# Performance work log

Hardware: AMD Instinct MI355X
Metric: run time of the kernel (lower is better)

Reference implementation:

```python
import jax, jax.numpy as jnp
import numpy as np

COMMITMENT_COST = 0.25


def setup_inputs() -> dict:
    key = jax.random.key(0)
    k1, k2 = jax.random.split(key)
    x = jax.random.normal(k1, (4, 64, 32, 32, 32), dtype=jnp.float32)
    weight = jax.random.normal(k2, (512, 64), dtype=jnp.float32)
    return {"x": x, "weight": weight}


def reference(x, weight):
    b, c, h, w, d = x.shape  # c == embed_dim
    # [b, h, w, d, c] -> [N, c]
    flat = jnp.transpose(x, (0, 2, 3, 4, 1)).reshape(-1, c)
    # squared L2 distances to each codebook vector: [N, n_embed]
    distances = (
        jnp.sum(flat * flat, axis=1, keepdims=True)
        - 2.0 * (flat @ weight.T)
        + jnp.sum(weight * weight, axis=1)
    )
    embed_idx_flat = jnp.argmin(distances, axis=1)  # == argmax(-distances)
    embed_idx = embed_idx_flat.reshape(b, h, w, d)
    # gather codebook rows and move embed dim back to channel position
    quantized = jnp.transpose(weight[embed_idx], (0, 4, 1, 2, 3))  # [b, c, h, w, d]
    latent_loss = COMMITMENT_COST * jnp.mean(
        (jax.lax.stop_gradient(quantized) - x) ** 2
    )
    quantized_st = jax.lax.stop_gradient(quantized - x) + x
    return quantized_st, embed_idx, latent_loss
```

## Files before the change

kernel.cpp:

```cpp
#include <hip/hip_runtime.h>
#include <hip/hip_bf16.h>

#define HWD      32768
#define NC       64
#define NE       512
#define OUT_IDX  8388608
#define OUT_LOSS 8519680

#define WS_WSQ_F   16
#define WS_SLOT_F  528
#define WS_WP_B    4096
#define WS_NEEDED  200704

typedef __attribute__((ext_vector_type(8))) short bf16x8;
typedef __attribute__((ext_vector_type(4))) float f32x4;

__device__ inline unsigned short bf16_rne(float v) {
    unsigned u = __builtin_bit_cast(unsigned, v);
    return (unsigned short)((u + 0x7FFFu + ((u >> 16) & 1u)) >> 16);
}
__device__ inline float bf16_f(unsigned short s) {
    return __builtin_bit_cast(float, (unsigned)s << 16);
}
__device__ inline void split3(float v, unsigned short& h, unsigned short& m,
                              unsigned short& l) {
    h = bf16_rne(v);
    float r1 = v - bf16_f(h);
    m = bf16_rne(r1);
    float r2 = r1 - bf16_f(m);
    l = bf16_rne(r2);
}

__global__ __launch_bounds__(256) void vq_prep(
    const float* __restrict__ w, float* __restrict__ ws)
{
    const int gtid = blockIdx.x * 256 + threadIdx.x;
    if (gtid == 0) { ws[0] = 0.f; ((unsigned*)ws)[1] = 0u; }
    if (gtid < 256) ws[WS_SLOT_F + gtid] = 0.f;
    if (gtid < NE) {
        const float4* row = (const float4*)(w + (size_t)gtid * NC);
        float s0 = 0.f, s1 = 0.f, s2 = 0.f, s3 = 0.f;
#pragma unroll
        for (int k = 0; k < 16; ++k) {
            float4 v = row[k];
            s0 = fmaf(v.x, v.x, s0); s1 = fmaf(v.y, v.y, s1);
            s2 = fmaf(v.z, v.z, s2); s3 = fmaf(v.w, v.w, s3);
        }
        ws[WS_WSQ_F + gtid] = (s0 + s1) + (s2 + s3);
    }
    const int lane_s = gtid & 63;
    int t = gtid >> 6;
    const int plane = t % 3; t /= 3;
    const int kc = t & 1;
    const int ct = t >> 1;
    const int code = ct * 16 + (lane_s & 15);
    const int kb   = kc * 32 + (lane_s >> 4) * 8;
    const float* src = w + (size_t)code * NC + kb;
    unsigned short o[8];
#pragma unroll
    for (int j = 0; j < 8; ++j) {
        unsigned short h, m, l;
        split3(src[j], h, m, l);
        o[j] = (plane == 0) ? h : (plane == 1) ? m : l;
    }
    unsigned short* dst = (unsigned short*)((char*)ws + WS_WP_B) + (size_t)gtid * 8;
#pragma unroll
    for (int j = 0; j < 8; ++j) dst[j] = o[j];
}

__device__ __forceinline__ void tileUpdPt(const bf16x8 (&Apt)[2][3],
                                          const bf16x8 (&B)[2][3],
                                          const float wsq, const int ct,
                                          const int lanelo,
                                          float (&best)[4], int (&bidx)[4])
{
    f32x4 acc = {0.f, 0.f, 0.f, 0.f};
    acc = __builtin_amdgcn_mfma_f32_16x16x32_bf16(Apt[0][2], B[0][0], acc, 0, 0, 0);
    acc = __builtin_amdgcn_mfma_f32_16x16x32_bf16(Apt[1][2], B[1][0], acc, 0, 0, 0);
    acc = __builtin_amdgcn_mfma_f32_16x16x32_bf16(Apt[0][1], B[0][1], acc, 0, 0, 0);
    acc = __builtin_amdgcn_mfma_f32_16x16x32_bf16(Apt[1][1], B[1][1], acc, 0, 0, 0);
    acc = __builtin_amdgcn_mfma_f32_16x16x32_bf16(Apt[0][0], B[0][2], acc, 0, 0, 0);
    acc = __builtin_amdgcn_mfma_f32_16x16x32_bf16(Apt[1][0], B[1][2], acc, 0, 0, 0);
    acc = __builtin_amdgcn_mfma_f32_16x16x32_bf16(Apt[0][1], B[0][0], acc, 0, 0, 0);
    acc = __builtin_amdgcn_mfma_f32_16x16x32_bf16(Apt[1][1], B[1][0], acc, 0, 0, 0);
    acc = __builtin_amdgcn_mfma_f32_16x16x32_bf16(Apt[0][0], B[0][1], acc, 0, 0, 0);
    acc = __builtin_amdgcn_mfma_f32_16x16x32_bf16(Apt[1][0], B[1][1], acc, 0, 0, 0);
    acc = __builtin_amdgcn_mfma_f32_16x16x32_bf16(Apt[0][0], B[0][0], acc, 0, 0, 0);
    acc = __builtin_amdgcn_mfma_f32_16x16x32_bf16(Apt[1][0], B[1][0], acc, 0, 0, 0);
#pragma unroll
    for (int r = 0; r < 4; ++r) {
        const float d = fmaf(-2.f, acc[r], wsq);
        if (d < best[r]) { best[r] = d; bidx[r] = ct * 16 + lanelo; }
    }
}

__global__ __launch_bounds__(256, 2) void vq_argmin(
    const float* __restrict__ x, float* __restrict__ ws,
    float* __restrict__ out)
{
    __shared__ int   idx_sh[256];
    __shared__ __align__(16) char Bsh[4][6144];
    __shared__ float wsq_sh[NE];

    const int tid    = threadIdx.x;
    const int wv     = tid >> 6;
    const int lane   = tid & 63;
    const int lanelo = lane & 15;
    const int quad   = lane >> 4;
    const int posB   = blockIdx.x * 256;
    const int b      = posB >> 15;
    const int hwdB   = posB & (HWD - 1);
    const size_t xoff = (size_t)b * NC * HWD + hwdB;
    const int wpos   = wv * 64;

    const char*  wpB  = (const char*)ws + WS_WP_B;
    const float* wsqp = ws + WS_WSQ_F;

    auto stageB = [&](int t, int bsel) {
#pragma unroll
        for (int cc = 0; cc < 2; ++cc) {
            const int c = wv + 4 * cc;
            if (c < 6) {
                const char* g = wpB + ((size_t)(t * 6 + c) * 64 + lane) * 16;
                void* l = &Bsh[bsel][c * 1024];
                __builtin_amdgcn_global_load_lds(
                    (const __attribute__((address_space(1))) unsigned*)g,
                    (__attribute__((address_space(3))) unsigned*)l, 16, 0, 0);
            }
        }
    };

    stageB(0, 0);
    stageB(1, 1);
    { wsq_sh[tid] = wsqp[tid]; wsq_sh[tid + 256] = wsqp[tid + 256]; }

    bf16x8 A[4][2][3];
#pragma unroll
    for (int pt = 0; pt < 4; ++pt) {
#pragma unroll
        for (int kc = 0; kc < 2; ++kc) {
            bf16x8 fh, fm, fl;
#pragma unroll
            for (int j = 0; j < 8; ++j) {
                const int k = kc * 32 + quad * 8 + j;
                const float v = x[xoff + (size_t)k * HWD + wpos + pt * 16 + lanelo];
                unsigned short h, m, l;
                split3(v, h, m, l);
                fh[j] = (short)h; fm[j] = (short)m; fl[j] = (short)l;
            }
            A[pt][kc][0] = fh; A[pt][kc][1] = fm; A[pt][kc][2] = fl;
        }
    }

    float best[4][4];
    int   bidx[4][4];
#pragma unroll
    for (int pt = 0; pt < 4; ++pt)
#pragma unroll
        for (int r = 0; r < 4; ++r) { best[pt][r] = 3.402823466e38f; bidx[pt][r] = 0; }

    __syncthreads();

#pragma unroll 1
    for (int r = 0; r < 16; ++r) {
        const int base = (r & 1) * 2;
        if (r < 15) {
            stageB(2 * r + 2, base ^ 2);
            stageB(2 * r + 3, (base ^ 2) + 1);
        }
#pragma unroll
        for (int s = 0; s < 2; ++s) {
            const int t = 2 * r + s;
            bf16x8 B[2][3];
            const bf16x8* bb = (const bf16x8*)Bsh[base + s];
#pragma unroll
            for (int kc = 0; kc < 2; ++kc)
#pragma unroll
                for (int p = 0; p < 3; ++p)
                    B[kc][p] = bb[(kc * 3 + p) * 64 + lane];
            const float wsq_c = wsq_sh[t * 16 + lanelo];
#pragma unroll
            for (int pt = 0; pt < 4; ++pt)
                tileUpdPt(A[pt], B, wsq_c, t, lanelo, best[pt], bidx[pt]);
        }
        __syncthreads();
    }

#pragma unroll
    for (int pt = 0; pt < 4; ++pt)
#pragma unroll
        for (int r = 0; r < 4; ++r) {
            float d = best[pt][r]; int i = bidx[pt][r];
#pragma unroll
            for (int mlane = 1; mlane <= 8; mlane <<= 1) {
                const float d2 = __shfl_xor(d, mlane);
                const int   i2 = __shfl_xor(i, mlane);
                if (d2 < d || (d2 == d && i2 < i)) { d = d2; i = i2; }
            }
            if (lanelo == 0)
                idx_sh[wpos + pt * 16 + quad * 4 + r] = i;
        }
    __syncthreads();

    out[OUT_IDX + posB + tid] = (float)idx_sh[tid];
}

__global__ __launch_bounds__(256, 8) void vq_epilogue(
    const float* __restrict__ x, const float* __restrict__ w,
    float* __restrict__ ws, float* __restrict__ out)
{
    __shared__ float q_t[64 * 68];
    __shared__ int   idx_sh[64];
    __shared__ float wred[4];

    const int tid  = threadIdx.x;
    const int posB = blockIdx.x * 64;
    const int b    = posB >> 15;
    const int hwdB = posB & (HWD - 1);
    const size_t xoff = (size_t)b * NC * HWD + hwdB;

    if (tid < 64) idx_sh[tid] = (int)out[OUT_IDX + posB + tid];
    __syncthreads();

#pragma unroll
    for (int it = 0; it < 16; ++it) {
        const int e = it * 256 + tid;
        const int r = e >> 6, c = e & 63;
        q_t[c * 68 + r] = w[(size_t)idx_sh[r] * NC + c];
    }
    __syncthreads();

    float lsum = 0.f;
#pragma unroll
    for (int it = 0; it < 4; ++it) {
        const int s  = it * 256 + tid;
        const int c  = s >> 4;
        const int p0 = (s & 15) * 4;
        const size_t off = xoff + (size_t)c * HWD + p0;
        const float4 xv = *(const float4*)(x + off);
        const float4 qv = *(const float4*)(q_t + c * 68 + p0);
        const float dx = qv.x - xv.x, dy = qv.y - xv.y;
        const float dz = qv.z - xv.z, dw = qv.w - xv.w;
        lsum = fmaf(dx, dx, lsum); lsum = fmaf(dy, dy, lsum);
        lsum = fmaf(dz, dz, lsum); lsum = fmaf(dw, dw, lsum);
        float4 ov;
        ov.x = dx + xv.x; ov.y = dy + xv.y;
        ov.z = dz + xv.z; ov.w = dw + xv.w;
        *(float4*)(out + off) = ov;
    }

#pragma unroll
    for (int off = 32; off >= 1; off >>= 1) lsum += __shfl_down(lsum, off);
    if ((tid & 63) == 0) wred[tid >> 6] = lsum;
    __syncthreads();
    if (tid == 0)
        atomicAdd(ws + WS_SLOT_F + (blockIdx.x & 255),
                  (wred[0] + wred[1]) + (wred[2] + wred[3]));
}

__global__ __launch_bounds__(64) void vq_loss_fin(
    const float* __restrict__ ws, float* __restrict__ out)
{
    const int lane = threadIdx.x;
    float s = (ws[WS_SLOT_F + lane]       + ws[WS_SLOT_F + lane + 64]) +
              (ws[WS_SLOT_F + lane + 128] + ws[WS_SLOT_F + lane + 192]);
#pragma unroll
    for (int off = 32; off >= 1; off >>= 1) s += __shfl_down(s, off);
    if (lane == 0) out[OUT_LOSS] = 0.25f * s / 8388608.0f;
}

__global__ __launch_bounds__(256, 2) void vq_fused_fb(
    const float* __restrict__ x, const float* __restrict__ w,
    float* __restrict__ out, float* __restrict__ loss_acc)
{
    __shared__ float lw[256 * NC];
    __shared__ float wsq[256];
    __shared__ float wred[4];
    const int tid = threadIdx.x;
    const int n0  = blockIdx.x * 512;
    const int b   = n0 >> 15;
    const int hwd = (n0 & (HWD - 1)) + tid;
    const float* xp = x + (size_t)b * NC * HWD + hwd;
    float xr0[NC], xr1[NC];
#pragma unroll
    for (int c = 0; c < NC; ++c) { xr0[c] = xp[(size_t)c * HWD]; xr1[c] = xp[(size_t)c * HWD + 256]; }
    float xsq0 = 0.f, xsq1 = 0.f;
#pragma unroll
    for (int c = 0; c < NC; ++c) { xsq0 = fmaf(xr0[c], xr0[c], xsq0); xsq1 = fmaf(xr1[c], xr1[c], xsq1); }
    float best0 = 3.402823466e38f, best1 = 3.402823466e38f;
    int bi0 = 0, bi1 = 0;
    for (int pass = 0; pass < 2; ++pass) {
        if (pass) __syncthreads();
        const float4* wt = (const float4*)(w + pass * 256 * NC);
        float4* l4 = (float4*)lw;
#pragma unroll
        for (int k = 0; k < 16; ++k) l4[tid + k * 256] = wt[tid + k * 256];
        {
            const float4* row = wt + tid * 16;
            float s0 = 0.f, s1 = 0.f, s2 = 0.f, s3 = 0.f;
#pragma unroll
            for (int k = 0; k < 16; ++k) {
                float4 v = row[k];
                s0 = fmaf(v.x, v.x, s0); s1 = fmaf(v.y, v.y, s1);
                s2 = fmaf(v.z, v.z, s2); s3 = fmaf(v.w, v.w, s3);
            }
            wsq[tid] = (s0 + s1) + (s2 + s3);
        }
        __syncthreads();
#pragma unroll 2
        for (int e = 0; e < 256; ++e) {
            const float4* row = (const float4*)(lw + e * NC);
            float a0 = 0.f, a1 = 0.f, c0 = 0.f, c1 = 0.f;
#pragma unroll
            for (int k = 0; k < 16; ++k) {
                float4 v = row[k];
                a0 = fmaf(xr0[4 * k + 0], v.x, a0); a1 = fmaf(xr0[4 * k + 1], v.y, a1);
                a0 = fmaf(xr0[4 * k + 2], v.z, a0); a1 = fmaf(xr0[4 * k + 3], v.w, a1);
                c0 = fmaf(xr1[4 * k + 0], v.x, c0); c1 = fmaf(xr1[4 * k + 1], v.y, c1);
                c0 = fmaf(xr1[4 * k + 2], v.z, c0); c1 = fmaf(xr1[4 * k + 3], v.w, c1);
            }
            const float d0 = (xsq0 - 2.f * (a0 + a1)) + wsq[e];
            const float d1 = (xsq1 - 2.f * (c0 + c1)) + wsq[e];
            const int ge = pass * 256 + e;
            if (d0 < best0) { best0 = d0; bi0 = ge; }
            if (d1 < best1) { best1 = d1; bi1 = ge; }
        }
    }
    float* o0 = out + (size_t)b * NC * HWD + hwd;
    float lsum = 0.f;
    const float4* r0 = (const float4*)(w + bi0 * NC);
    const float4* r1 = (const float4*)(w + bi1 * NC);
#pragma unroll
    for (int k = 0; k < 16; ++k) {
        float4 q0 = r0[k], q1 = r1[k];
        float qv0[4] = { q0.x, q0.y, q0.z, q0.w };
        float qv1[4] = { q1.x, q1.y, q1.z, q1.w };
#pragma unroll
        for (int j = 0; j < 4; ++j) {
            const int c = 4 * k + j;
            const float dv0 = qv0[j] - xr0[c];
            const float dv1 = qv1[j] - xr1[c];
            lsum = fmaf(dv0, dv0, lsum); lsum = fmaf(dv1, dv1, lsum);
            o0[(size_t)c * HWD] = dv0 + xr0[c];
            o0[(size_t)c * HWD + 256] = dv1 + xr1[c];
        }
    }
    const int n = b * HWD + hwd;
    out[OUT_IDX + n] = (float)bi0;
    out[OUT_IDX + n + 256] = (float)bi1;
#pragma unroll
    for (int off = 32; off >= 1; off >>= 1) lsum += __shfl_down(lsum, off);
    if ((tid & 63) == 0) wred[tid >> 6] = lsum;
    __syncthreads();
    if (tid == 0) atomicAdd(loss_acc, (wred[0] + wred[1]) + (wred[2] + wred[3]));
}

__global__ void vq_loss_fin_fb(const float* __restrict__ acc, float* __restrict__ out)
{
    out[OUT_LOSS] = 0.25f * acc[0] / 8388608.0f;
}

extern "C" void kernel_launch(void* const* d_in, const int* in_sizes, int n_in,
                              void* d_out, int out_size, void* d_ws, size_t ws_size,
                              hipStream_t stream)
{
    const float* x = (const float*)d_in[0];
    const float* w = (const float*)d_in[1];
    float* out = (float*)d_out;
    float* ws  = (float*)d_ws;

    if (ws_size >= WS_NEEDED) {
        vq_prep<<<48, 256, 0, stream>>>(w, ws);
        vq_argmin<<<512, 256, 0, stream>>>(x, ws, out);
        vq_epilogue<<<2048, 256, 0, stream>>>(x, w, ws, out);
        vq_loss_fin<<<1, 64, 0, stream>>>(ws, out);
    } else {
        hipMemsetAsync(d_ws, 0, sizeof(float), stream);
        vq_fused_fb<<<256, 256, 0, stream>>>(x, w, out, ws);
        vq_loss_fin_fb<<<1, 1, 0, stream>>>(ws, out);
    }
}
```

Baseline: 136.0 us.

## Load codebook fragments directly to registers and interleave MFMA chains across point tiles

Drops the LDS staging of the split-bf16 codebook (global_load_lds with double buffering and per-iteration barriers). Each wave now loads its B fragments and wsq straight from global/L2 into registers, software-pipelined one code tile ahead. The MFMA loop is also restructured so that four independent accumulator chains (one per point tile) are interleaved, which hides MFMA dependency latency. In exchange there are more redundant global loads per wave, since every wave fetches the same codebook data, and register pressure rises under launch bounds of two blocks per SM.

New measurement: 135.3 us (median of 3 runs). No clear change (-0.5%).

```diff
diff --git a/kernel.cpp b/kernel.cpp
--- a/kernel.cpp
+++ b/kernel.cpp
@@ -68,39 +68,53 @@
     for (int j = 0; j < 8; ++j) dst[j] = o[j];
 }
 
-__device__ __forceinline__ void tileUpdPt(const bf16x8 (&Apt)[2][3],
-                                          const bf16x8 (&B)[2][3],
-                                          const float wsq, const int ct,
-                                          const int lanelo,
-                                          float (&best)[4], int (&bidx)[4])
-{
-    f32x4 acc = {0.f, 0.f, 0.f, 0.f};
-    acc = __builtin_amdgcn_mfma_f32_16x16x32_bf16(Apt[0][2], B[0][0], acc, 0, 0, 0);
-    acc = __builtin_amdgcn_mfma_f32_16x16x32_bf16(Apt[1][2], B[1][0], acc, 0, 0, 0);
-    acc = __builtin_amdgcn_mfma_f32_16x16x32_bf16(Apt[0][1], B[0][1], acc, 0, 0, 0);
-    acc = __builtin_amdgcn_mfma_f32_16x16x32_bf16(Apt[1][1], B[1][1], acc, 0, 0, 0);
-    acc = __builtin_amdgcn_mfma_f32_16x16x32_bf16(Apt[0][0], B[0][2], acc, 0, 0, 0);
-    acc = __builtin_amdgcn_mfma_f32_16x16x32_bf16(Apt[1][0], B[1][2], acc, 0, 0, 0);
-    acc = __builtin_amdgcn_mfma_f32_16x16x32_bf16(Apt[0][1], B[0][0], acc, 0, 0, 0);
-    acc = __builtin_amdgcn_mfma_f32_16x16x32_bf16(Apt[1][1], B[1][0], acc, 0, 0, 0);
-    acc = __builtin_amdgcn_mfma_f32_16x16x32_bf16(Apt[0][0], B[0][1], acc, 0, 0, 0);
-    acc = __builtin_amdgcn_mfma_f32_16x16x32_bf16(Apt[1][0], B[1][1], acc, 0, 0, 0);
-    acc = __builtin_amdgcn_mfma_f32_16x16x32_bf16(Apt[0][0], B[0][0], acc, 0, 0, 0);
-    acc = __builtin_amdgcn_mfma_f32_16x16x32_bf16(Apt[1][0], B[1][0], acc, 0, 0, 0);
-#pragma unroll
-    for (int r = 0; r < 4; ++r) {
-        const float d = fmaf(-2.f, acc[r], wsq);
-        if (d < best[r]) { best[r] = d; bidx[r] = ct * 16 + lanelo; }
-    }
+__device__ __forceinline__ void loadB(const bf16x8* __restrict__ wp,
+                                      const float* __restrict__ wsqp,
+                                      const int ct, const int lane,
+                                      const int lanelo,
+                                      bf16x8 (&B)[2][3], float& wsq)
+{
+#pragma unroll
+    for (int kc = 0; kc < 2; ++kc)
+#pragma unroll
+        for (int p = 0; p < 3; ++p)
+            B[kc][p] = wp[(size_t)((ct * 2 + kc) * 3 + p) * 64 + lane];
+    wsq = wsqp[ct * 16 + lanelo];
+}
+
+__device__ __forceinline__ void tileUpd4(const bf16x8 (&A)[4][2][3],
+                                         const bf16x8 (&B)[2][3],
+                                         const float wsq, const int ct,
+                                         const int lanelo,
+                                         float (&best)[4][4], int (&bidx)[4][4])
+{
+    constexpr int AP[6] = {2, 1, 0, 1, 0, 0};
+    constexpr int BP[6] = {0, 1, 2, 0, 1, 0};
+    f32x4 acc[4];
+#pragma unroll
+    for (int pt = 0; pt < 4; ++pt) acc[pt] = (f32x4){0.f, 0.f, 0.f, 0.f};
+#pragma unroll
+    for (int s = 0; s < 12; ++s) {
+        const int kc = s & 1, ap = AP[s >> 1], bp = BP[s >> 1];
+#pragma unroll
+        for (int pt = 0; pt < 4; ++pt)
+            acc[pt] = __builtin_amdgcn_mfma_f32_16x16x32_bf16(
+                A[pt][kc][ap], B[kc][bp], acc[pt], 0, 0, 0);
+    }
+#pragma unroll
+    for (int pt = 0; pt < 4; ++pt)
+#pragma unroll
+        for (int r = 0; r < 4; ++r) {
+            const float d = fmaf(-2.f, acc[pt][r], wsq);
+            if (d < best[pt][r]) { best[pt][r] = d; bidx[pt][r] = ct * 16 + lanelo; }
+        }
 }
 
 __global__ __launch_bounds__(256, 2) void vq_argmin(
     const float* __restrict__ x, float* __restrict__ ws,
     float* __restrict__ out)
 {
-    __shared__ int   idx_sh[256];
-    __shared__ __align__(16) char Bsh[4][6144];
-    __shared__ float wsq_sh[NE];
+    __shared__ int idx_sh[256];
 
     const int tid    = threadIdx.x;
     const int wv     = tid >> 6;
@@ -113,26 +127,12 @@
     const size_t xoff = (size_t)b * NC * HWD + hwdB;
     const int wpos   = wv * 64;
 
-    const char*  wpB  = (const char*)ws + WS_WP_B;
-    const float* wsqp = ws + WS_WSQ_F;
-
-    auto stageB = [&](int t, int bsel) {
-#pragma unroll
-        for (int cc = 0; cc < 2; ++cc) {
-            const int c = wv + 4 * cc;
-            if (c < 6) {
-                const char* g = wpB + ((size_t)(t * 6 + c) * 64 + lane) * 16;
-                void* l = &Bsh[bsel][c * 1024];
-                __builtin_amdgcn_global_load_lds(
-                    (const __attribute__((address_space(1))) unsigned*)g,
-                    (__attribute__((address_space(3))) unsigned*)l, 16, 0, 0);
-            }
-        }
-    };
-
-    stageB(0, 0);
-    stageB(1, 1);
-    { wsq_sh[tid] = wsqp[tid]; wsq_sh[tid + 256] = wsqp[tid + 256]; }
+    const bf16x8* wp   = (const bf16x8*)((const char*)ws + WS_WP_B);
+    const float*  wsqp = ws + WS_WSQ_F;
+
+    bf16x8 B0[2][3], B1[2][3];
+    float  w0, w1;
+    loadB(wp, wsqp, 0, lane, lanelo, B0, w0);
 
     bf16x8 A[4][2][3];
 #pragma unroll
@@ -159,31 +159,13 @@
 #pragma unroll
         for (int r = 0; r < 4; ++r) { best[pt][r] = 3.402823466e38f; bidx[pt][r] = 0; }
 
-    __syncthreads();
-
 #pragma unroll 1
     for (int r = 0; r < 16; ++r) {
-        const int base = (r & 1) * 2;
-        if (r < 15) {
-            stageB(2 * r + 2, base ^ 2);
-            stageB(2 * r + 3, (base ^ 2) + 1);
-        }
-#pragma unroll
-        for (int s = 0; s < 2; ++s) {
-            const int t = 2 * r + s;
-            bf16x8 B[2][3];
-            const bf16x8* bb = (const bf16x8*)Bsh[base + s];
-#pragma unroll
-            for (int kc = 0; kc < 2; ++kc)
-#pragma unroll
-                for (int p = 0; p < 3; ++p)
-                    B[kc][p] = bb[(kc * 3 + p) * 64 + lane];
-            const float wsq_c = wsq_sh[t * 16 + lanelo];
-#pragma unroll
-            for (int pt = 0; pt < 4; ++pt)
-                tileUpdPt(A[pt], B, wsq_c, t, lanelo, best[pt], bidx[pt]);
-        }
-        __syncthreads();
+        const int ce = r * 2;
+        loadB(wp, wsqp, ce + 1, lane, lanelo, B1, w1);
+        tileUpd4(A, B0, w0, ce, lanelo, best, bidx);
+        loadB(wp, wsqp, (ce + 2) & 31, lane, lanelo, B0, w0);
+        tileUpd4(A, B1, w1, ce + 1, lanelo, best, bidx);
     }
 
 #pragma unroll
```
